# Performance work log

Measured on AMD Instinct MI355X. Metric: run time of the kernel, lower is better.

The kernel has to match this reference:

```python
import jax, jax.numpy as jnp
import numpy as np

N_NODES = 80000
N_EDGES = 1280000
D_NODE = 128
D_EDGE = 32
D_HID = 64
NEG_SLOPE = 0.2


def setup_inputs() -> dict:
    key = jax.random.key(0)
    ks = jax.random.split(key, 9)
    return {
        "node_features": jax.random.normal(ks[0], (N_NODES, D_NODE), dtype=jnp.float32),
        "edge_features": jax.random.normal(ks[1], (N_EDGES, D_EDGE), dtype=jnp.float32),
        "edge_index": jax.random.randint(ks[2], (2, N_EDGES), 0, N_NODES, dtype=jnp.int64),
        # params: w (node Linear), edgew (edge Linear), attn (3*hid -> 1)
        "w_w": jax.random.normal(ks[3], (D_NODE, D_HID), dtype=jnp.float32) / np.sqrt(D_NODE),
        "w_b": jax.random.normal(ks[4], (D_HID,), dtype=jnp.float32) * 0.01,
        "ew_w": jax.random.normal(ks[5], (D_EDGE, D_HID), dtype=jnp.float32) / np.sqrt(D_EDGE),
        "ew_b": jax.random.normal(ks[6], (D_HID,), dtype=jnp.float32) * 0.01,
        "a_w": jax.random.normal(ks[7], (3 * D_HID, 1), dtype=jnp.float32) / np.sqrt(3 * D_HID),
        "a_b": jax.random.normal(ks[8], (1,), dtype=jnp.float32) * 0.01,
    }


def reference(node_features, edge_features, edge_index, w_w, w_b, ew_w, ew_b, a_w, a_b):
    n_nodes = node_features.shape[0]
    h = node_features @ w_w + w_b              # [N, H]
    edge_h = edge_features @ ew_w + ew_b       # [E, H]
    tgt = edge_index[0]                        # target (softmax group) nodes i
    nbr = edge_index[1]                        # neighbor nodes j
    h_i = h[tgt]                               # [E, H] gather
    h_j = h[nbr]                               # [E, H] gather
    h_concat = jnp.concatenate([h_i, h_j, edge_h], axis=-1)  # [E, 3H]
    eij = jax.nn.leaky_relu(h_concat @ a_w + a_b, negative_slope=NEG_SLOPE)  # [E, 1]
    # scatter-softmax over edges grouped by target node (numerically stable)
    seg_max = jax.ops.segment_max(eij, tgt, num_segments=n_nodes)            # [N, 1]
    ex = jnp.exp(eij - seg_max[tgt])
    seg_sum = jax.ops.segment_sum(ex, tgt, num_segments=n_nodes)             # [N, 1]
    alpha = ex / seg_sum[tgt]                                                # [E, 1]
    # (dropout omitted for deterministic reference)
    message = alpha * h_j                                                    # [E, H]
    out = jax.ops.segment_sum(message, tgt, num_segments=n_nodes)            # [N, H]
    return jax.nn.elu(out)
```

## Files before the change

### kernel.cpp

```cpp
#include <hip/hip_runtime.h>
#include <math.h>

#define N_NODES 80000
#define N_EDGES 1280000
#define D_NODE  128
#define D_EDGE  32
#define D_HID   64
#define NEG_SLOPE 0.2f
#define NB 313
#define CAP 4608
#define BCNT_STRIDE 16
#define EB_BLK 512
#define EB_CHUNK 2048
#define EB_NCHUNK (N_EDGES / EB_CHUNK)

__device__ inline float waveReduceSum(float v) {
    #pragma unroll
    for (int o = 32; o > 0; o >>= 1) v += __shfl_xor(v, o);
    return v;
}
__device__ inline unsigned short f2bf(float f) {
    unsigned u = __float_as_uint(f);
    return (unsigned short)((u + 0x7FFF + ((u >> 16) & 1)) >> 16);
}
__device__ inline float bf2f(unsigned short v) {
    return __uint_as_float(((unsigned)v) << 16);
}

__global__ __launch_bounds__(256) void node_kernel(
        const float* __restrict__ nf, const float* __restrict__ w_w,
        const float* __restrict__ w_b, const float* __restrict__ a_w,
        unsigned short* __restrict__ hb, float* __restrict__ s1, float* __restrict__ s2) {
    __shared__ float Ws[D_HID * D_NODE];
    __shared__ float Xs[32][D_NODE];
    for (int i = threadIdx.x; i < D_NODE * D_HID; i += 256) {
        int k = i >> 6, d = i & 63;
        Ws[d * D_NODE + (((k >> 2) ^ (d & 7)) << 2) + (k & 3)] = w_w[i];
    }
    int lane = threadIdx.x & 63;
    int wv   = threadIdx.x >> 6;
    float wb = w_b[lane];
    float a1 = a_w[lane];
    float a2 = a_w[D_HID + lane];
    const float* wrow = &Ws[lane * D_NODE];
    const int nTiles = N_NODES / 32;
    for (int tile = blockIdx.x; tile < nTiles; tile += gridDim.x) {
        int n0 = tile * 32;
        __syncthreads();
        {
            const float4* src = (const float4*)(nf + (size_t)n0 * D_NODE);
            float4* dst = (float4*)&Xs[0][0];
            #pragma unroll
            for (int j = 0; j < 4; ++j)
                dst[threadIdx.x + 256 * j] = src[threadIdx.x + 256 * j];
        }
        __syncthreads();
        float acc[8] = {0.f, 0.f, 0.f, 0.f, 0.f, 0.f, 0.f, 0.f};
        const float* xs = &Xs[wv * 8][0];
        #pragma unroll 4
        for (int k4 = 0; k4 < 32; ++k4) {
            float4 w = *(const float4*)&wrow[(k4 ^ (lane & 7)) << 2];
            #pragma unroll
            for (int n = 0; n < 8; ++n) {
                float4 x = *(const float4*)&xs[n * D_NODE + (k4 << 2)];
                acc[n] += w.x * x.x + w.y * x.y + w.z * x.z + w.w * x.w;
            }
        }
        #pragma unroll
        for (int n = 0; n < 8; ++n) {
            int node = n0 + wv * 8 + n;
            float hv = acc[n] + wb;
            hb[(size_t)node * D_HID + lane] = f2bf(hv);
            float r1 = waveReduceSum(hv * a1);
            float r2 = waveReduceSum(hv * a2);
            if (lane == 0) { s1[node] = r1; s2[node] = r2; }
        }
    }
}

__global__ __launch_bounds__(EB_BLK) void edge_bin_kernel(
        const float* __restrict__ ef, const int* __restrict__ eidx,
        const float* __restrict__ s2v,
        const float* __restrict__ ew_w, const float* __restrict__ ew_b,
        const float* __restrict__ a_w, const float* __restrict__ a_b,
        int* __restrict__ bcnt, int2* __restrict__ binned) {
    __shared__ float cs[D_EDGE];
    __shared__ float bes;
    __shared__ int hist[NB], gbase[NB], rank[NB];
    __shared__ float sq [EB_CHUNK];
    __shared__ int   stg[EB_CHUNK];
    __shared__ int   snb[EB_CHUNK];
    int tid = threadIdx.x;
    if (tid < D_EDGE) {
        float s = 0.f;
        #pragma unroll
        for (int d = 0; d < D_HID; ++d) s += ew_w[tid * D_HID + d] * a_w[2 * D_HID + d];
        cs[tid] = s;
    } else if (tid == D_EDGE) {
        float s = 0.f;
        #pragma unroll
        for (int d = 0; d < D_HID; ++d) s += ew_b[d] * a_w[2 * D_HID + d];
        bes = s + a_b[0];
    }
    int qd = tid >> 2;
    int j  = tid & 3;
    for (int c = blockIdx.x; c < EB_NCHUNK; c += gridDim.x) {
        for (int i = tid; i < NB; i += EB_BLK) { hist[i] = 0; rank[i] = 0; }
        __syncthreads();
        int e0 = c * EB_CHUNK;
        #pragma unroll
        for (int k = 0; k < 4; ++k) {
            int idx = k * EB_BLK + tid;
            int e = e0 + idx;
            int tg = eidx[e];
            int nb = eidx[N_EDGES + e];
            stg[idx] = tg;
            snb[idx] = nb;
            sq [idx] = bes + s2v[nb];
            atomicAdd(&hist[tg >> 8], 1);
        }
        __syncthreads();
        #pragma unroll 2
        for (int rr = 0; rr < EB_CHUNK / 128; ++rr) {
            int idx = rr * 128 + qd;
            int e = e0 + idx;
            const float4* f4 = (const float4*)ef;
            float4 fa = f4[(size_t)e * 8 + j];
            float4 fb = f4[(size_t)e * 8 + 4 + j];
            const float4 c1 = *(const float4*)&cs[j * 4];
            const float4 c2 = *(const float4*)&cs[16 + j * 4];
            float p = fa.x * c1.x + fa.y * c1.y + fa.z * c1.z + fa.w * c1.w
                    + fb.x * c2.x + fb.y * c2.y + fb.z * c2.z + fb.w * c2.w;
            p += __shfl_xor(p, 1);
            p += __shfl_xor(p, 2);
            if (j == 0) sq[idx] += p;
        }
        __syncthreads();
        for (int i = tid; i < NB; i += EB_BLK) {
            int cc = hist[i];
            if (cc) gbase[i] = i * CAP + atomicAdd(&bcnt[i * BCNT_STRIDE], cc);
        }
        __syncthreads();
        #pragma unroll
        for (int k = 0; k < 4; ++k) {
            int idx = k * EB_BLK + tid;
            int tg = stg[idx];
            int b  = tg >> 8;
            int r  = atomicAdd(&rank[b], 1);
            binned[gbase[b] + r] = make_int2(((tg & 255) << 17) | snb[idx],
                                             __float_as_int(sq[idx]));
        }
        __syncthreads();
    }
}

__global__ __launch_bounds__(1024) void bucket_accum_kernel(
        const int* __restrict__ bcnt, const int2* __restrict__ binned,
        const float* __restrict__ s1, const unsigned short* __restrict__ hb,
        float* __restrict__ out) {
    __shared__ int nhist[256], buf[256], sbase[256], ncur[256];
    __shared__ int2 slab[CAP];
    int tid = threadIdx.x;
    int b = blockIdx.x;
    int in0 = b * CAP;
    int cnt = bcnt[b * BCNT_STRIDE];
    if (tid < 256) nhist[tid] = 0;
    __syncthreads();
    for (int i = tid; i < cnt; i += 1024)
        atomicAdd(&nhist[binned[in0 + i].x >> 17], 1);
    __syncthreads();
    if (tid < 256) buf[tid] = nhist[tid];
    __syncthreads();
    for (int ofs = 1; ofs < 256; ofs <<= 1) {
        int t = 0;
        if (tid < 256 && tid >= ofs) t = buf[tid - ofs];
        __syncthreads();
        if (tid < 256) buf[tid] += t;
        __syncthreads();
    }
    if (tid < 256) {
        int excl = buf[tid] - nhist[tid];
        sbase[tid] = excl;
        ncur[tid]  = excl;
    }
    __syncthreads();
    for (int i = tid; i < cnt; i += 1024) {
        int2 p = binned[in0 + i];
        int r = atomicAdd(&ncur[p.x >> 17], 1);
        slab[r] = make_int2(p.x & 0x1FFFF, p.y);
    }
    __syncthreads();
    int grp = tid >> 4;
    int li  = tid & 15;
    int wl  = ((tid & 63) >> 4) << 4;
    for (int nl = grp; nl < 256; nl += 64) {
        int node = b * 256 + nl;
        if (node >= N_NODES) break;
        int base = sbase[nl];
        int cn   = nhist[nl];
        float s1i = s1[node];
        float ax = 0.f, ay = 0.f, az = 0.f, aw = 0.f, sumex = 0.f;
        for (int c0 = 0; c0 < cn; c0 += 16) {
            int i = c0 + li;
            int nc = min(16, cn - c0);
            float exv = 0.f; int nbv = 0;
            if (i < cn) {
                int2 p = slab[base + i];
                nbv = p.x;
                float s = s1i + __int_as_float(p.y);
                s = (s > 0.f) ? s : NEG_SLOPE * s;
                exv = __expf(s);
            }
            sumex += exv;
            for (int j = 0; j < nc; ++j) {
                float w  = __shfl(exv, wl + j);
                int   nb = __shfl(nbv, wl + j);
                uint2 v = *(const uint2*)&hb[(size_t)nb * D_HID + li * 4];
                ax += w * bf2f((unsigned short)(v.x & 0xFFFF));
                ay += w * bf2f((unsigned short)(v.x >> 16));
                az += w * bf2f((unsigned short)(v.y & 0xFFFF));
                aw += w * bf2f((unsigned short)(v.y >> 16));
            }
        }
        #pragma unroll
        for (int o = 8; o > 0; o >>= 1) sumex += __shfl_xor(sumex, o);
        float4 o4;
        if (cn == 0) {
            o4 = make_float4(0.f, 0.f, 0.f, 0.f);
        } else {
            o4.x = ax / sumex; o4.y = ay / sumex; o4.z = az / sumex; o4.w = aw / sumex;
            o4.x = (o4.x > 0.f) ? o4.x : (__expf(o4.x) - 1.f);
            o4.y = (o4.y > 0.f) ? o4.y : (__expf(o4.y) - 1.f);
            o4.z = (o4.z > 0.f) ? o4.z : (__expf(o4.z) - 1.f);
            o4.w = (o4.w > 0.f) ? o4.w : (__expf(o4.w) - 1.f);
        }
        ((float4*)out)[(size_t)node * 16 + li] = o4;
    }
}

extern "C" void kernel_launch(void* const* d_in, const int* in_sizes, int n_in,
                              void* d_out, int out_size, void* d_ws, size_t ws_size,
                              hipStream_t stream) {
    const float* nf   = (const float*)d_in[0];
    const float* ef   = (const float*)d_in[1];
    const int*   eidx = (const int*)d_in[2];
    const float* w_w  = (const float*)d_in[3];
    const float* w_b  = (const float*)d_in[4];
    const float* ew_w = (const float*)d_in[5];
    const float* ew_b = (const float*)d_in[6];
    const float* a_w  = (const float*)d_in[7];
    const float* a_b  = (const float*)d_in[8];
    float* out = (float*)d_out;

    char* ws = (char*)d_ws;
    size_t o = 0;
    auto alloc = [&](size_t bytes) -> void* {
        void* p = ws + o;
        o = (o + bytes + 255) & ~(size_t)255;
        return p;
    };
    unsigned short* hb  = (unsigned short*)alloc((size_t)N_NODES * D_HID * 2);
    float* s1       = (float*)alloc((size_t)N_NODES * 4);
    float* s2       = (float*)alloc((size_t)N_NODES * 4);
    int*   bcnt     = (int*)alloc((size_t)NB * BCNT_STRIDE * 4);
    int2*  binned   = (int2*)alloc((size_t)NB * CAP * 8);

    hipMemsetAsync(bcnt, 0, (size_t)NB * BCNT_STRIDE * 4, stream);

    node_kernel<<<1250, 256, 0, stream>>>(nf, w_w, w_b, a_w, hb, s1, s2);
    edge_bin_kernel<<<EB_NCHUNK, EB_BLK, 0, stream>>>(ef, eidx, s2, ew_w, ew_b, a_w, a_b, bcnt, binned);
    bucket_accum_kernel<<<NB, 1024, 0, stream>>>(bcnt, binned, s1, hb, out);
}
```

Baseline: 149.2 us.

## Stage binned edges in shared memory by bucket before coalesced global scatter

The edge binning kernel now keeps target and neighbour indices in registers instead of shared arrays. It runs a block-wide prefix scan over the bucket histogram and places each edge's packed record in a bucket-sorted shared staging buffer along with its global destination. The global writes then happen in a second pass, so consecutive threads write consecutive slots within each bucket instead of scattering randomly. The cost is a 9-step scan with barriers per chunk and extra shared-memory traffic.

```diff
diff --git a/kernel.cpp b/kernel.cpp
--- a/kernel.cpp
+++ b/kernel.cpp
@@ -87,9 +87,10 @@
     __shared__ float cs[D_EDGE];
     __shared__ float bes;
     __shared__ int hist[NB], gbase[NB], rank[NB];
+    __shared__ int scanbuf[512];
     __shared__ float sq [EB_CHUNK];
-    __shared__ int   stg[EB_CHUNK];
-    __shared__ int   snb[EB_CHUNK];
+    __shared__ int2  sval[EB_CHUNK];
+    __shared__ int   sdst[EB_CHUNK];
     int tid = threadIdx.x;
     if (tid < D_EDGE) {
         float s = 0.f;
@@ -108,16 +109,15 @@
         for (int i = tid; i < NB; i += EB_BLK) { hist[i] = 0; rank[i] = 0; }
         __syncthreads();
         int e0 = c * EB_CHUNK;
+        int RT[4], RN[4];
         #pragma unroll
         for (int k = 0; k < 4; ++k) {
             int idx = k * EB_BLK + tid;
             int e = e0 + idx;
-            int tg = eidx[e];
-            int nb = eidx[N_EDGES + e];
-            stg[idx] = tg;
-            snb[idx] = nb;
-            sq [idx] = bes + s2v[nb];
-            atomicAdd(&hist[tg >> 8], 1);
+            RT[k] = eidx[e];
+            RN[k] = eidx[N_EDGES + e];
+            sq[idx] = bes + s2v[RN[k]];
+            atomicAdd(&hist[RT[k] >> 8], 1);
         }
         __syncthreads();
         #pragma unroll 2
@@ -140,15 +140,30 @@
             int cc = hist[i];
             if (cc) gbase[i] = i * CAP + atomicAdd(&bcnt[i * BCNT_STRIDE], cc);
         }
-        __syncthreads();
+        scanbuf[tid] = (tid < NB) ? hist[tid] : 0;
+        __syncthreads();
+        for (int ofs = 1; ofs < 512; ofs <<= 1) {
+            int t = (tid >= (unsigned)ofs) ? scanbuf[tid - ofs] : 0;
+            __syncthreads();
+            scanbuf[tid] += t;
+            __syncthreads();
+        }
         #pragma unroll
         for (int k = 0; k < 4; ++k) {
             int idx = k * EB_BLK + tid;
-            int tg = stg[idx];
+            int tg = RT[k];
             int b  = tg >> 8;
             int r  = atomicAdd(&rank[b], 1);
-            binned[gbase[b] + r] = make_int2(((tg & 255) << 17) | snb[idx],
-                                             __float_as_int(sq[idx]));
+            int slot = scanbuf[b] - hist[b] + r;
+            sval[slot] = make_int2(((tg & 255) << 17) | RN[k],
+                                   __float_as_int(sq[idx]));
+            sdst[slot] = gbase[b] + r;
+        }
+        __syncthreads();
+        #pragma unroll
+        for (int k = 0; k < 4; ++k) {
+            int i = k * EB_BLK + tid;
+            binned[sdst[i]] = sval[i];
         }
         __syncthreads();
     }
@@ -212,9 +227,9 @@
                 exv = __expf(s);
             }
             sumex += exv;
-            for (int j = 0; j < nc; ++j) {
-                float w  = __shfl(exv, wl + j);
-                int   nb = __shfl(nbv, wl + j);
+            for (int jj = 0; jj < nc; ++jj) {
+                float w  = __shfl(exv, wl + jj);
+                int   nb = __shfl(nbv, wl + jj);
                 uint2 v = *(const uint2*)&hb[(size_t)nb * D_HID + li * 4];
                 ax += w * bf2f((unsigned short)(v.x & 0xFFFF));
                 ay += w * bf2f((unsigned short)(v.x >> 16));
```

Result: no change. 147.2 us (-1.3%).
